# Performance work log

Measured on AMD Instinct MI355X. Metric: run time of the kernel, lower is better.

## Reference

```python
import jax, jax.numpy as jnp
import numpy as np

ALPHA = 0.2  # leaky relu slope
DEPTH = 3
MAX_REF = 10
MAX_DIR = 32

def leaky(x):
    return jnp.where(x >= 0, x, ALPHA * x)

def setup_inputs() -> dict:
    key = jax.random.key(0)
    ks = jax.random.split(key, 9)
    N, F_IN, F_OUT = 100000, 128, 128
    h = jax.random.normal(ks[0], (N, F_IN), dtype=jnp.float32)
    W_ref = jax.random.normal(ks[1], (F_IN, F_OUT), dtype=jnp.float32) * 0.1
    a_ref = jax.random.normal(ks[2], (2 * F_OUT, 1), dtype=jnp.float32) * 0.1
    W_dir = jax.random.normal(ks[3], (F_IN, F_OUT), dtype=jnp.float32) * 0.1
    a_dir = jax.random.normal(ks[4], (2 * F_OUT, 1), dtype=jnp.float32) * 0.1
    ref_neighbors = jax.random.randint(ks[5], (N, DEPTH + 1, MAX_REF), 0, N)
    ref_counts = jax.random.randint(ks[6], (N, DEPTH + 1), 0, MAX_REF + 1)
    dir_neighbors = jax.random.randint(ks[7], (N, MAX_DIR), 0, N)
    dir_counts = jax.random.randint(ks[8], (N,), 1, MAX_DIR + 1)
    return {"h": h, "W_ref": W_ref, "a_ref": a_ref, "W_dir": W_dir, "a_dir": a_dir,
            "ref_neighbors": ref_neighbors, "ref_counts": ref_counts,
            "dir_neighbors": dir_neighbors, "dir_counts": dir_counts}

def _forward_ref(h, W_ref, a_ref, ref_neighbors, ref_counts):
    Wh = h @ W_ref                                  # [N, F]
    F_ = Wh.shape[1]
    # mean of (up to 10) neighbor features per (node, depth); empty -> zeros
    nbr = Wh[ref_neighbors]                         # [N, D+1, 10, F]
    slot = jnp.arange(MAX_REF)[None, None, :]
    valid = slot < ref_counts[:, :, None]           # [N, D+1, 10]
    cnt = jnp.maximum(ref_counts, 1).astype(Wh.dtype)  # avoid div by 0
    f_ref = jnp.einsum('ndkf,ndk->ndf', nbr, valid.astype(Wh.dtype)) / cnt[:, :, None]  # [N, D+1, F]
    # attention score: leaky(cat(Wh[node], f_ref[d]) @ a_ref)
    a_self, a_nbr = a_ref[:F_, 0], a_ref[F_:, 0]
    e = leaky(Wh @ a_self[:, None] + f_ref @ a_nbr)  # [N,1]+[N,D+1] -> [N, D+1]
    alpha = jax.nn.softmax(e, axis=-1)
    out = jnp.einsum('ndf,nd->nf', f_ref, alpha)
    return jax.nn.sigmoid(out)

def _forward_dir(h, W_dir, a_dir, dir_neighbors, dir_counts):
    Wh = h @ W_dir                                  # [N, F]
    F_ = Wh.shape[1]
    nbr = Wh[dir_neighbors]                         # [N, K, F]
    a_self, a_nbr = a_dir[:F_, 0], a_dir[F_:, 0]
    e = leaky((Wh @ a_self)[:, None] + nbr @ a_nbr)  # [N, K]
    valid = jnp.arange(MAX_DIR)[None, :] < dir_counts[:, None]
    e = jnp.where(valid, e, -jnp.inf)
    alpha = jax.nn.softmax(e, axis=-1)
    out = jnp.einsum('nkf,nk->nf', nbr, alpha)
    return jax.nn.sigmoid(out)

def reference(h, W_ref, a_ref, W_dir, a_dir, ref_neighbors, ref_counts, dir_neighbors, dir_counts):
    h_ref = _forward_ref(h, W_ref, a_ref, ref_neighbors, ref_counts)
    h_dir = _forward_dir(h, W_dir, a_dir, dir_neighbors, dir_counts)
    return (h_ref + h_dir) / 2  # mode='mean'
```

## Files before the change

### kernel.cpp

```cpp
#include <hip/hip_runtime.h>

typedef __attribute__((ext_vector_type(8))) short s16x8;
typedef __attribute__((ext_vector_type(4))) float f32x4;
typedef __attribute__((ext_vector_type(2))) float f32x2;

#define F 128

__device__ __forceinline__ unsigned short f2bf(float f) {
    unsigned int u = __float_as_uint(f);
    u = (u + 0x7fffu + ((u >> 16) & 1u)) >> 16;
    return (unsigned short)u;
}
__device__ __forceinline__ float bflo(unsigned int u) { return __uint_as_float(u << 16); }
__device__ __forceinline__ float bfhi(unsigned int u) { return __uint_as_float(u & 0xffff0000u); }
__device__ __forceinline__ float leaky(float x) { return x >= 0.f ? x : 0.2f * x; }
__device__ __forceinline__ float sigmoidf(float x) { return 1.f / (1.f + __expf(-x)); }

#define SWZ16(row, b) ((b) ^ (((row) & 7) << 4))

#define WAVE_LDS_FENCE() do { \
    asm volatile("s_waitcnt lgkmcnt(0)" ::: "memory"); \
    __builtin_amdgcn_sched_barrier(0); \
} while (0)

#define AWAIT_VM0() do { \
    asm volatile("s_waitcnt vmcnt(0)" ::: "memory"); \
    __builtin_amdgcn_sched_barrier(0); \
} while (0)

__device__ __forceinline__ void glds16(void* lds, const void* g) {
    __builtin_amdgcn_global_load_lds(
        (const __attribute__((address_space(1))) unsigned int*)g,
        (__attribute__((address_space(3))) unsigned int*)lds,
        16, 0, 0);
}

__device__ __forceinline__ void pkfma(f32x2& a, f32x2 p, f32x2 cc) {
    asm("v_pk_fma_f32 %0, %1, %2, %0" : "+v"(a) : "v"(p), "v"(cc));
}
__device__ __forceinline__ void accrow(f32x2* a4, uint2 u, float c) {
    f32x2 cc; cc[0] = c; cc[1] = c;
    pkfma(a4[0], __builtin_amdgcn_cvt_pk_f32_fp8((int)u.x, false), cc);
    pkfma(a4[1], __builtin_amdgcn_cvt_pk_f32_fp8((int)u.x, true),  cc);
    pkfma(a4[2], __builtin_amdgcn_cvt_pk_f32_fp8((int)u.y, false), cc);
    pkfma(a4[3], __builtin_amdgcn_cvt_pk_f32_fp8((int)u.y, true),  cc);
}

__global__ __launch_bounds__(256) void prep_w(const float* __restrict__ wRef,
                                              const float* __restrict__ wDir,
                                              unsigned short* __restrict__ wT) {
    int i = blockIdx.x * 256 + threadIdx.x;
    int m = i >> 14;
    int rr = i & 16383;
    int k = rr >> 7;
    int c = rr & 127;
    const float* W = m ? wDir : wRef;
    wT[m * 16384 + c * 128 + (k ^ (((c & 7) << 3)))] = f2bf(W[k * 128 + c]);
}

__device__ __forceinline__ void epi(const f32x4* acc, unsigned char* cb,
                                    int rowBase, int w, int r, int g, int lane, int N,
                                    const float* __restrict__ aVec,
                                    unsigned char* __restrict__ wh,
                                    float* __restrict__ sArr, float* __restrict__ tArr) {
    float ps[4] = {0.f, 0.f, 0.f, 0.f}, pt[4] = {0.f, 0.f, 0.f, 0.f};
#pragma unroll
    for (int ct = 0; ct < 8; ++ct) {
        int c = ct * 16 + r;
        float As = aVec[c], At = aVec[128 + c];
#pragma unroll
        for (int q = 0; q < 4; ++q) { ps[q] += acc[ct][q] * As; pt[q] += acc[ct][q] * At; }
    }
#pragma unroll
    for (int off = 1; off <= 8; off <<= 1) {
#pragma unroll
        for (int q = 0; q < 4; ++q) {
            ps[q] += __shfl_xor(ps[q], off);
            pt[q] += __shfl_xor(pt[q], off);
        }
    }
    if (r == 0) {
#pragma unroll
        for (int q = 0; q < 4; ++q) {
            int row = rowBase + w * 16 + g * 4 + q;
            if (row < N) { sArr[row] = ps[q]; tArr[row] = pt[q]; }
        }
    }
#pragma unroll
    for (int ct = 0; ct < 8; ++ct) {
#pragma unroll
        for (int q = 0; q < 4; ++q) {
            int lrow = g * 4 + q;
            int xb = (ct * 16 + r) * 2;
            *(unsigned short*)(cb + lrow * 256 + SWZ16(lrow, xb)) = f2bf(acc[ct][q]);
        }
    }
#pragma unroll
    for (int i = 0; i < 4; ++i) {
        int off = i * 1024 + lane * 16;
        int lrow = off >> 8, x = off & 255;
        uint4 v = *(const uint4*)(cb + lrow * 256 + SWZ16(lrow, x));
        int pk0 = __builtin_amdgcn_cvt_pk_fp8_f32(bflo(v.x), bfhi(v.x), 0, false);
        pk0 = __builtin_amdgcn_cvt_pk_fp8_f32(bflo(v.y), bfhi(v.y), pk0, true);
        int pk1 = __builtin_amdgcn_cvt_pk_fp8_f32(bflo(v.z), bfhi(v.z), 0, false);
        pk1 = __builtin_amdgcn_cvt_pk_fp8_f32(bflo(v.w), bfhi(v.w), pk1, true);
        int grow = rowBase + w * 16 + lrow;
        if (grow < N) *(uint2*)(wh + (size_t)grow * 128 + (x >> 1)) = make_uint2((unsigned)pk0, (unsigned)pk1);
    }
}

__global__ __launch_bounds__(256) void gemm_wh(const float* __restrict__ h,
                                               const unsigned short* __restrict__ wT,
                                               const float* __restrict__ aRefG,
                                               const float* __restrict__ aDirG,
                                               unsigned char* __restrict__ whRef,
                                               unsigned char* __restrict__ whDir,
                                               float* __restrict__ sRef, float* __restrict__ tRef,
                                               float* __restrict__ sDir, float* __restrict__ tDir,
                                               int N) {
    __shared__ unsigned char lds[49152];
    const int tid = threadIdx.x;
    const int lane = tid & 63, w = tid >> 6;
    const int r = lane & 15, g = lane >> 4;
    const int rowBase = blockIdx.x * 64;

#pragma unroll
    for (int it = 0; it < 8; ++it) {
        int lin = it * 4096 + tid * 16;
        glds16(lds + 16384 + lin, (const char*)wT + lin);
    }
    float4 av[4][2];
#pragma unroll
    for (int it = 0; it < 4; ++it) {
        int lin = it * 4096 + tid * 16;
        int arow = lin >> 8, x = lin & 255;
        int grow = min(rowBase + arow, N - 1);
        const char* src = (const char*)h + (size_t)grow * 512 + x * 2;
        av[it][0] = *(const float4*)(src);
        av[it][1] = *(const float4*)(src + 16);
    }
#pragma unroll
    for (int it = 0; it < 4; ++it) {
        int lin = it * 4096 + tid * 16;
        int arow = lin >> 8, x = lin & 255;
        s16x8 a;
        a[0] = (short)f2bf(av[it][0].x); a[1] = (short)f2bf(av[it][0].y);
        a[2] = (short)f2bf(av[it][0].z); a[3] = (short)f2bf(av[it][0].w);
        a[4] = (short)f2bf(av[it][1].x); a[5] = (short)f2bf(av[it][1].y);
        a[6] = (short)f2bf(av[it][1].z); a[7] = (short)f2bf(av[it][1].w);
        *(s16x8*)(lds + arow * 256 + SWZ16(arow, x)) = a;
    }
    __syncthreads();

    s16x8 afr[4];
    {
        const int arow = w * 16 + r;
#pragma unroll
        for (int kt = 0; kt < 4; ++kt)
            afr[kt] = *(const s16x8*)(lds + arow * 256 + SWZ16(arow, kt * 64 + g * 16));
    }
    unsigned char* cb = lds + w * 4096;

    {
        f32x4 acc[8];
#pragma unroll
        for (int ct = 0; ct < 8; ++ct) acc[ct] = (f32x4){0.f, 0.f, 0.f, 0.f};
#pragma unroll
        for (int kt = 0; kt < 4; ++kt) {
#pragma unroll
            for (int ct = 0; ct < 8; ++ct) {
                int c = ct * 16 + r;
                s16x8 b = *(const s16x8*)(lds + 16384 + c * 256 + SWZ16(c, kt * 64 + g * 16));
                acc[ct] = __builtin_amdgcn_mfma_f32_16x16x32_bf16(afr[kt], b, acc[ct], 0, 0, 0);
            }
        }
        epi(acc, cb, rowBase, w, r, g, lane, N, aRefG, whRef, sRef, tRef);
    }
    __syncthreads();
#pragma unroll
    for (int it = 0; it < 8; ++it) {
        int lin = it * 4096 + tid * 16;
        glds16(lds + 16384 + lin, (const char*)wT + 32768 + lin);
    }
    __syncthreads();
    {
        f32x4 acc[8];
#pragma unroll
        for (int ct = 0; ct < 8; ++ct) acc[ct] = (f32x4){0.f, 0.f, 0.f, 0.f};
#pragma unroll
        for (int kt = 0; kt < 4; ++kt) {
#pragma unroll
            for (int ct = 0; ct < 8; ++ct) {
                int c = ct * 16 + r;
                s16x8 b = *(const s16x8*)(lds + 16384 + c * 256 + SWZ16(c, kt * 64 + g * 16));
                acc[ct] = __builtin_amdgcn_mfma_f32_16x16x32_bf16(afr[kt], b, acc[ct], 0, 0, 0);
            }
        }
        epi(acc, cb, rowBase, w, r, g, lane, N, aDirG, whDir, sDir, tDir);
    }
}

__global__ __launch_bounds__(256) void gather_attn(
    const unsigned char* __restrict__ whRef, const unsigned char* __restrict__ whDir,
    const float* __restrict__ sRef, const float* __restrict__ tRef,
    const float* __restrict__ sDir, const float* __restrict__ tDir,
    const int* __restrict__ refNbr, const int* __restrict__ refCnt,
    const int* __restrict__ dirNbr, const int* __restrict__ dirCnt,
    float* __restrict__ out, int N) {
    __shared__ unsigned char s_stage[4][9216];
    __shared__ int   s_idx[4][72];
    __shared__ float s_coef[4][72];

    const int wid = threadIdx.x >> 6;
    const int lane = threadIdx.x & 63;
    const int q = lane >> 4, hl16 = lane & 15;
    const int d = lane >> 4, kk = lane & 15;
    const int n_raw = blockIdx.x * 4 + wid;
    const int n = min(n_raw, N - 1);
    unsigned char* stg = s_stage[wid];

    s_idx[wid][lane] = 0;
    if (lane < 8) s_idx[wid][64 + lane] = 0;

    int cnt = refCnt[n * 4 + d];
    int idxR = (kk < 10) ? refNbr[(size_t)n * 40 + d * 10 + kk] : 0;
    int dcnt = dirCnt[n];
    int idxD = (lane < 32) ? dirNbr[(size_t)n * 32 + lane] : 0;
    float sR = sRef[n], sD = sDir[n];

    bool validR = kk < cnt;
    bool validD = (lane < 32) && (lane < dcnt);
    float rc = 1.f / (float)max(cnt, 1);
    unsigned long long mask = __ballot(validR);
    int pos = (int)__popcll(mask & ((1ull << lane) - 1ull));
    int Lr = (int)__popcll(mask);
    WAVE_LDS_FENCE();
    if (validR) s_idx[wid][pos] = idxR;
    if (validD) s_idx[wid][40 + lane] = idxD;

    float tv = validR ? tRef[idxR] : 0.f;
    float tD = validD ? tDir[idxD] : 0.f;
    WAVE_LDS_FENCE();

    const int nR8 = (Lr + 7) >> 3;
    const int nD8 = (dcnt + 7) >> 3;
    const int sub = (lane >> 3);
    const int seg = (lane & 7) << 4;
    for (int j = 0; j < nR8; ++j) {
        int row = s_idx[wid][j * 8 + sub];
        glds16(stg + j * 1024 + lane * 16,
               whRef + ((size_t)(unsigned)row << 7) + seg);
    }
    for (int j = 0; j < nD8; ++j) {
        int row = s_idx[wid][40 + j * 8 + sub];
        glds16(stg + 5120 + j * 1024 + lane * 16,
               whDir + ((size_t)(unsigned)row << 7) + seg);
    }
    __builtin_amdgcn_sched_barrier(0);

    float sum = tv;
    sum += __shfl_xor(sum, 1); sum += __shfl_xor(sum, 2);
    sum += __shfl_xor(sum, 4); sum += __shfl_xor(sum, 8);
    float e = leaky(sR + sum * rc);
    float mx = fmaxf(e, __shfl_xor(e, 16)); mx = fmaxf(mx, __shfl_xor(mx, 32));
    float wgt = __expf(e - mx);
    float den = wgt + __shfl_xor(wgt, 16); den += __shfl_xor(den, 32);
    if (validR) s_coef[wid][pos] = wgt / den * rc;

    float eD = validD ? leaky(sD + tD) : -1e30f;
    float mD = eD;
#pragma unroll
    for (int off = 16; off; off >>= 1) mD = fmaxf(mD, __shfl_xor(mD, off, 32));
    float wD = validD ? __expf(eD - mD) : 0.f;
    float dD = wD;
#pragma unroll
    for (int off = 16; off; off >>= 1) dD += __shfl_xor(dD, off, 32);
    if (validD) s_coef[wid][40 + lane] = wD / dD;
    WAVE_LDS_FENCE();

    AWAIT_VM0();

    f32x2 aR[4] = {{0.f,0.f},{0.f,0.f},{0.f,0.f},{0.f,0.f}};
    {
        int mR = (Lr + 3) >> 2;
        for (int j = 0; j < mR; ++j) {
            int e2 = j * 4 + q;
            if (e2 < Lr) {
                uint2 u = *(const uint2*)(stg + e2 * 128 + (hl16 << 3));
                accrow(aR, u, s_coef[wid][e2]);
            }
        }
    }
    f32x2 aD4[4] = {{0.f,0.f},{0.f,0.f},{0.f,0.f},{0.f,0.f}};
    {
        int mD4 = (dcnt + 3) >> 2;
        for (int j = 0; j < mD4; ++j) {
            int e2 = j * 4 + q;
            if (e2 < dcnt) {
                uint2 u = *(const uint2*)(stg + 5120 + e2 * 128 + (hl16 << 3));
                accrow(aD4, u, s_coef[wid][40 + e2]);
            }
        }
    }

    float accR[8], accD[8];
#pragma unroll
    for (int j = 0; j < 4; ++j) {
        accR[2*j] = aR[j][0]; accR[2*j+1] = aR[j][1];
        accD[2*j] = aD4[j][0]; accD[2*j+1] = aD4[j][1];
    }
#pragma unroll
    for (int j = 0; j < 8; ++j) {
        accR[j] += __shfl_xor(accR[j], 16); accR[j] += __shfl_xor(accR[j], 32);
        accD[j] += __shfl_xor(accD[j], 16); accD[j] += __shfl_xor(accD[j], 32);
    }
    if (n_raw < N && q == 0) {
        float o[8];
#pragma unroll
        for (int j = 0; j < 8; ++j) o[j] = 0.5f * (sigmoidf(accR[j]) + sigmoidf(accD[j]));
        float4* dst = (float4*)(out + (size_t)n * F + hl16 * 8);
        dst[0] = make_float4(o[0], o[1], o[2], o[3]);
        dst[1] = make_float4(o[4], o[5], o[6], o[7]);
    }
}

extern "C" void kernel_launch(void* const* d_in, const int* in_sizes, int n_in,
                              void* d_out, int out_size, void* d_ws, size_t ws_size,
                              hipStream_t stream) {
    const float* h    = (const float*)d_in[0];
    const float* Wref = (const float*)d_in[1];
    const float* aRef = (const float*)d_in[2];
    const float* Wdir = (const float*)d_in[3];
    const float* aDir = (const float*)d_in[4];
    const int* refNbr = (const int*)d_in[5];
    const int* refCnt = (const int*)d_in[6];
    const int* dirNbr = (const int*)d_in[7];
    const int* dirCnt = (const int*)d_in[8];
    float* out = (float*)d_out;
    const int N = in_sizes[0] / F;

    const size_t NF = (size_t)N * F;
    unsigned char* whRef = (unsigned char*)d_ws;
    unsigned char* whDir = whRef + NF;
    float* sRef = (float*)(whDir + NF);
    float* tRef = sRef + N;
    float* sDir = tRef + N;
    float* tDir = sDir + N;
    unsigned short* wT = (unsigned short*)(tDir + N);

    prep_w<<<128, 256, 0, stream>>>(Wref, Wdir, wT);
    gemm_wh<<<(N + 63) / 64, 256, 0, stream>>>(h, wT, aRef, aDir, whRef, whDir,
                                               sRef, tRef, sDir, tDir, N);
    gather_attn<<<(N + 3) / 4, 256, 0, stream>>>(whRef, whDir, sRef, tRef, sDir, tDir,
                                                 refNbr, refCnt, dirNbr, dirCnt, out, N);
}
```

Measured before the change: 288.8 us.

## Gather neighbor rows directly into registers instead of staging through LDS

```diff
diff --git a/kernel.cpp b/kernel.cpp
--- a/kernel.cpp
+++ b/kernel.cpp
@@ -20,11 +20,6 @@
 
 #define WAVE_LDS_FENCE() do { \
     asm volatile("s_waitcnt lgkmcnt(0)" ::: "memory"); \
-    __builtin_amdgcn_sched_barrier(0); \
-} while (0)
-
-#define AWAIT_VM0() do { \
-    asm volatile("s_waitcnt vmcnt(0)" ::: "memory"); \
     __builtin_amdgcn_sched_barrier(0); \
 } while (0)
 
@@ -38,12 +33,16 @@
 __device__ __forceinline__ void pkfma(f32x2& a, f32x2 p, f32x2 cc) {
     asm("v_pk_fma_f32 %0, %1, %2, %0" : "+v"(a) : "v"(p), "v"(cc));
 }
-__device__ __forceinline__ void accrow(f32x2* a4, uint2 u, float c) {
+__device__ __forceinline__ void accrow16(f32x2* a8, uint4 u, float c) {
     f32x2 cc; cc[0] = c; cc[1] = c;
-    pkfma(a4[0], __builtin_amdgcn_cvt_pk_f32_fp8((int)u.x, false), cc);
-    pkfma(a4[1], __builtin_amdgcn_cvt_pk_f32_fp8((int)u.x, true),  cc);
-    pkfma(a4[2], __builtin_amdgcn_cvt_pk_f32_fp8((int)u.y, false), cc);
-    pkfma(a4[3], __builtin_amdgcn_cvt_pk_f32_fp8((int)u.y, true),  cc);
+    pkfma(a8[0], __builtin_amdgcn_cvt_pk_f32_fp8((int)u.x, false), cc);
+    pkfma(a8[1], __builtin_amdgcn_cvt_pk_f32_fp8((int)u.x, true),  cc);
+    pkfma(a8[2], __builtin_amdgcn_cvt_pk_f32_fp8((int)u.y, false), cc);
+    pkfma(a8[3], __builtin_amdgcn_cvt_pk_f32_fp8((int)u.y, true),  cc);
+    pkfma(a8[4], __builtin_amdgcn_cvt_pk_f32_fp8((int)u.z, false), cc);
+    pkfma(a8[5], __builtin_amdgcn_cvt_pk_f32_fp8((int)u.z, true),  cc);
+    pkfma(a8[6], __builtin_amdgcn_cvt_pk_f32_fp8((int)u.w, false), cc);
+    pkfma(a8[7], __builtin_amdgcn_cvt_pk_f32_fp8((int)u.w, true),  cc);
 }
 
 __global__ __launch_bounds__(256) void prep_w(const float* __restrict__ wRef,
@@ -207,20 +206,15 @@
     const int* __restrict__ refNbr, const int* __restrict__ refCnt,
     const int* __restrict__ dirNbr, const int* __restrict__ dirCnt,
     float* __restrict__ out, int N) {
-    __shared__ unsigned char s_stage[4][9216];
     __shared__ int   s_idx[4][72];
     __shared__ float s_coef[4][72];
 
     const int wid = threadIdx.x >> 6;
     const int lane = threadIdx.x & 63;
-    const int q = lane >> 4, hl16 = lane & 15;
     const int d = lane >> 4, kk = lane & 15;
+    const int g8 = lane >> 3, l8 = lane & 7;
     const int n_raw = blockIdx.x * 4 + wid;
     const int n = min(n_raw, N - 1);
-    unsigned char* stg = s_stage[wid];
-
-    s_idx[wid][lane] = 0;
-    if (lane < 8) s_idx[wid][64 + lane] = 0;
 
     int cnt = refCnt[n * 4 + d];
     int idxR = (kk < 10) ? refNbr[(size_t)n * 40 + d * 10 + kk] : 0;
@@ -234,29 +228,11 @@
     unsigned long long mask = __ballot(validR);
     int pos = (int)__popcll(mask & ((1ull << lane) - 1ull));
     int Lr = (int)__popcll(mask);
-    WAVE_LDS_FENCE();
     if (validR) s_idx[wid][pos] = idxR;
-    if (validD) s_idx[wid][40 + lane] = idxD;
+    if (lane < 32) s_idx[wid][40 + lane] = idxD;
 
     float tv = validR ? tRef[idxR] : 0.f;
     float tD = validD ? tDir[idxD] : 0.f;
-    WAVE_LDS_FENCE();
-
-    const int nR8 = (Lr + 7) >> 3;
-    const int nD8 = (dcnt + 7) >> 3;
-    const int sub = (lane >> 3);
-    const int seg = (lane & 7) << 4;
-    for (int j = 0; j < nR8; ++j) {
-        int row = s_idx[wid][j * 8 + sub];
-        glds16(stg + j * 1024 + lane * 16,
-               whRef + ((size_t)(unsigned)row << 7) + seg);
-    }
-    for (int j = 0; j < nD8; ++j) {
-        int row = s_idx[wid][40 + j * 8 + sub];
-        glds16(stg + 5120 + j * 1024 + lane * 16,
-               whDir + ((size_t)(unsigned)row << 7) + seg);
-    }
-    __builtin_amdgcn_sched_barrier(0);
 
     float sum = tv;
     sum += __shfl_xor(sum, 1); sum += __shfl_xor(sum, 2);
@@ -278,49 +254,53 @@
     if (validD) s_coef[wid][40 + lane] = wD / dD;
     WAVE_LDS_FENCE();
 
-    AWAIT_VM0();
-
-    f32x2 aR[4] = {{0.f,0.f},{0.f,0.f},{0.f,0.f},{0.f,0.f}};
-    {
-        int mR = (Lr + 3) >> 2;
+    f32x2 aR[8] = {{0,0},{0,0},{0,0},{0,0},{0,0},{0,0},{0,0},{0,0}};
+    {
+        int mR = (Lr + 7) >> 3;
         for (int j = 0; j < mR; ++j) {
-            int e2 = j * 4 + q;
+            int e2 = j * 8 + g8;
             if (e2 < Lr) {
-                uint2 u = *(const uint2*)(stg + e2 * 128 + (hl16 << 3));
-                accrow(aR, u, s_coef[wid][e2]);
+                uint4 u = *(const uint4*)(whRef + ((size_t)(unsigned)s_idx[wid][e2] << 7) + (l8 << 4));
+                accrow16(aR, u, s_coef[wid][e2]);
             }
         }
     }
-    f32x2 aD4[4] = {{0.f,0.f},{0.f,0.f},{0.f,0.f},{0.f,0.f}};
-    {
-        int mD4 = (dcnt + 3) >> 2;
-        for (int j = 0; j < mD4; ++j) {
-            int e2 = j * 4 + q;
+    f32x2 aD8[8] = {{0,0},{0,0},{0,0},{0,0},{0,0},{0,0},{0,0},{0,0}};
+    {
+        int mDj = (dcnt + 7) >> 3;
+        for (int j = 0; j < mDj; ++j) {
+            int e2 = j * 8 + g8;
             if (e2 < dcnt) {
-                uint2 u = *(const uint2*)(stg + 5120 + e2 * 128 + (hl16 << 3));
-                accrow(aD4, u, s_coef[wid][40 + e2]);
+                uint4 u = *(const uint4*)(whDir + ((size_t)(unsigned)s_idx[wid][40 + e2] << 7) + (l8 << 4));
+                accrow16(aD8, u, s_coef[wid][40 + e2]);
             }
         }
     }
 
-    float accR[8], accD[8];
-#pragma unroll
-    for (int j = 0; j < 4; ++j) {
-        accR[2*j] = aR[j][0]; accR[2*j+1] = aR[j][1];
-        accD[2*j] = aD4[j][0]; accD[2*j+1] = aD4[j][1];
-    }
 #pragma unroll
     for (int j = 0; j < 8; ++j) {
-        accR[j] += __shfl_xor(accR[j], 16); accR[j] += __shfl_xor(accR[j], 32);
-        accD[j] += __shfl_xor(accD[j], 16); accD[j] += __shfl_xor(accD[j], 32);
-    }
-    if (n_raw < N && q == 0) {
-        float o[8];
-#pragma unroll
-        for (int j = 0; j < 8; ++j) o[j] = 0.5f * (sigmoidf(accR[j]) + sigmoidf(accD[j]));
-        float4* dst = (float4*)(out + (size_t)n * F + hl16 * 8);
-        dst[0] = make_float4(o[0], o[1], o[2], o[3]);
-        dst[1] = make_float4(o[4], o[5], o[6], o[7]);
+#pragma unroll
+        for (int c2 = 0; c2 < 2; ++c2) {
+            float vR = aR[j][c2], vD = aD8[j][c2];
+            vR += __shfl_xor(vR, 8);  vD += __shfl_xor(vD, 8);
+            vR += __shfl_xor(vR, 16); vD += __shfl_xor(vD, 16);
+            vR += __shfl_xor(vR, 32); vD += __shfl_xor(vD, 32);
+            aR[j][c2] = vR; aD8[j][c2] = vD;
+        }
+    }
+
+    if (n_raw < N && g8 == 0) {
+        float o[16];
+#pragma unroll
+        for (int j = 0; j < 8; ++j) {
+            o[2*j]   = 0.5f * (sigmoidf(aR[j][0]) + sigmoidf(aD8[j][0]));
+            o[2*j+1] = 0.5f * (sigmoidf(aR[j][1]) + sigmoidf(aD8[j][1]));
+        }
+        float4* dst = (float4*)(out + (size_t)n * F + l8 * 16);
+        dst[0] = make_float4(o[0],  o[1],  o[2],  o[3]);
+        dst[1] = make_float4(o[4],  o[5],  o[6],  o[7]);
+        dst[2] = make_float4(o[8],  o[9],  o[10], o[11]);
+        dst[3] = make_float4(o[12], o[13], o[14], o[15]);
     }
 }
 
```

After: 321.8 us. +11.4%, slower.
